# Optimization experiments

Measured on AMD Instinct MI355X. Metric: run time of the kernel, lower is better.

The kernel has to match this reference:

```python
import jax, jax.numpy as jnp
import numpy as np

N = 50000
E = 800000
NEG_SLOPE = 0.2  # PyG GATConv default


def _glorot(key, shape, scale=0.1):
    return jax.random.normal(key, shape, dtype=jnp.float32) * scale


def setup_inputs() -> dict:
    key = jax.random.key(0)
    ks = jax.random.split(key, 16)
    X = jax.random.normal(ks[0], (N, 128), dtype=jnp.float32)
    edge_index = jax.random.randint(ks[1], (2, E), 0, N, dtype=jnp.int64)
    edge_weight = jax.random.uniform(ks[2], (E,), dtype=jnp.float32)
    # GATConv layer params: W [in,out], att_src/att_dst [out], bias [out]
    W1, as1, ad1, b1 = _glorot(ks[3], (128, 128)), _glorot(ks[4], (128,)), _glorot(ks[5], (128,)), jnp.zeros((128,), jnp.float32)
    W2, as2, ad2, b2 = _glorot(ks[6], (128, 64)), _glorot(ks[7], (64,)), _glorot(ks[8], (64,)), jnp.zeros((64,), jnp.float32)
    W3, as3, ad3, b3 = _glorot(ks[9], (64, 32)), _glorot(ks[10], (32,)), _glorot(ks[11], (32,)), jnp.zeros((32,), jnp.float32)
    Wl, bl = _glorot(ks[12], (32, 1)), jnp.zeros((1,), jnp.float32)
    return {"X": X, "edge_index": edge_index, "edge_weight": edge_weight,
            "W1": W1, "as1": as1, "ad1": ad1, "b1": b1,
            "W2": W2, "as2": as2, "ad2": ad2, "b2": b2,
            "W3": W3, "as3": as3, "ad3": ad3, "b3": b3,
            "Wl": Wl, "bl": bl}


def gat_layer(x, src, dst, W, a_src, a_dst, b):
    # x: [N, in] -> h: [N, out]
    h = x @ W
    # per-node attention logits, gathered per edge
    alpha = jax.nn.leaky_relu((h * a_src).sum(-1)[src] + (h * a_dst).sum(-1)[dst], NEG_SLOPE)  # [E']
    # segment-softmax over incoming edges of each dst node
    amax = jax.ops.segment_max(alpha, dst, num_segments=N)
    ex = jnp.exp(alpha - amax[dst])
    denom = jax.ops.segment_sum(ex, dst, num_segments=N)
    w = ex / (denom[dst] + 1e-16)
    # scatter-add weighted messages
    out = jax.ops.segment_sum(h[src] * w[:, None], dst, num_segments=N)
    return out + b


def reference(X, edge_index, edge_weight, W1, as1, ad1, b1, W2, as2, ad2, b2, W3, as3, ad3, b3, Wl, bl):
    # GATConv add_self_loops=True: append self loops (static shape)
    loops = jnp.arange(N, dtype=edge_index.dtype)
    src = jnp.concatenate([edge_index[0], loops])
    dst = jnp.concatenate([edge_index[1], loops])
    # edge_weight is ignored by PyG GATConv when edge_dim is None (faithful)
    x = jax.nn.elu(gat_layer(X, src, dst, W1, as1, ad1, b1))
    x = jax.nn.elu(gat_layer(x, src, dst, W2, as2, ad2, b2))
    x = jax.nn.elu(gat_layer(x, src, dst, W3, as3, ad3, b3))
    x = x @ Wl + bl
    return jax.nn.sigmoid(x)[:, 0]
```

## Files before the change

kernel.cpp:

```cpp
#include <hip/hip_runtime.h>
#include <hip/hip_bf16.h>

typedef __attribute__((ext_vector_type(8))) short bf16x8;
typedef __attribute__((ext_vector_type(4))) float f32x4;

constexpr int NBMAX = 128;
constexpr int EPB   = 2048;
constexpr int CAP   = 12288;


__device__ __forceinline__ float bf2f(unsigned short u) {
    union { unsigned int i; float f; } c; c.i = ((unsigned int)u) << 16; return c.f;
}
__device__ __forceinline__ unsigned short f2bf(float f) {
    union { unsigned int i; float f; } c; c.f = f;
    unsigned int i = c.i;
    unsigned int r = (i + 0x7FFFu + ((i >> 16) & 1u)) >> 16;
    return (unsigned short)r;
}


__device__ __forceinline__ void pack_one(const float* __restrict__ W, int K, int OUT, int idx,
                                         unsigned short* __restrict__ hi, unsigned short* __restrict__ lo) {
    int KS = K >> 5;
    int lane = idx & 63;
    int rest = idx >> 6;
    int ks = rest % KS, ct = rest / KS;
    int m = lane & 15, kg = lane >> 4;
    size_t base = (size_t)idx * 8;
#pragma unroll
    for (int j = 0; j < 8; ++j) {
        float w = W[(size_t)(ks * 32 + kg * 8 + j) * OUT + ct * 16 + m];
        unsigned short h = f2bf(w);
        hi[base + j] = h;
        lo[base + j] = f2bf(w - bf2f(h));
    }
}

__global__ void pack_init(const float* __restrict__ W1, unsigned short* hi1, unsigned short* lo1,
                          const float* __restrict__ W2, unsigned short* hi2, unsigned short* lo2,
                          const float* __restrict__ W3, unsigned short* hi3, unsigned short* lo3,
                          int* __restrict__ cursor, int nb) {
    if (blockIdx.x < 13) {
        int idx = blockIdx.x * 256 + threadIdx.x;
        if (idx < 2048)               pack_one(W1, 128, 128, idx, hi1, lo1);
        else if (idx < 2048 + 1024)   pack_one(W2, 128,  64, idx - 2048, hi2, lo2);
        else if (idx < 2048 + 1280)   pack_one(W3,  64,  32, idx - 3072, hi3, lo3);
    } else {
        int t = threadIdx.x;
        if (t < nb) cursor[t] = t * CAP;
    }
}


__global__ __launch_bounds__(256) void bin_passA(const int* __restrict__ ei, int E, int N, int nb,
                                                 int* __restrict__ cursor,
                                                 unsigned int* __restrict__ stageG) {
    __shared__ int bcnt[NBMAX], bofs[NBMAX], gbase[NBMAX], bfill[NBMAX];
    __shared__ unsigned int stage[EPB];
    const int t = threadIdx.x;
    const int Et = E + N;
    const int e0 = blockIdx.x * EPB;
    const int ecnt = min(EPB, Et - e0);
    if (t < nb) { bcnt[t] = 0; bfill[t] = 0; }
    __syncthreads();
    unsigned int pk[8];
#pragma unroll
    for (int k = 0; k < 8; ++k) {
        int e = e0 + t + k * 256;
        pk[k] = 0xFFFFFFFFu;
        if (e < Et) {
            int s, d;
            if (e < E) { s = ei[e]; d = ei[E + e]; } else { s = d = e - E; }
            pk[k] = ((unsigned int)d << 16) | (unsigned int)s;
            atomicAdd(&bcnt[d >> 9], 1);
        }
    }
    __syncthreads();
    if (t == 0) {
        int run = 0;
        for (int i = 0; i < nb; ++i) { bofs[i] = run; run += bcnt[i]; }
    }
    __syncthreads();
    if (t < nb && bcnt[t] > 0) gbase[t] = atomicAdd(&cursor[t], bcnt[t]);
    __syncthreads();
#pragma unroll
    for (int k = 0; k < 8; ++k) {
        if (pk[k] != 0xFFFFFFFFu) {
            int b = pk[k] >> 25;
            int pos = bofs[b] + atomicAdd(&bfill[b], 1);
            stage[pos] = pk[k];
        }
    }
    __syncthreads();
    for (int i = t; i < ecnt; i += 256) {
        unsigned int p = stage[i];
        int b = p >> 25;
        stageG[(size_t)gbase[b] + (i - bofs[b])] = p;
    }
}


template <int K, int OUT>
__device__ __forceinline__ void gemm_body(const float* __restrict__ X,
                                          const unsigned short* __restrict__ Whi,
                                          const unsigned short* __restrict__ Wlo,
                                          const float* __restrict__ avs,
                                          const float* __restrict__ avd,
                                          unsigned short* __restrict__ Hb,
                                          float* __restrict__ asrc,
                                          float* __restrict__ adst, int N, int waveIdx) {
    constexpr int CT = OUT / 16, KS = K / 32;
    const int lane = threadIdx.x & 63;
    const int row0 = waveIdx << 4;
    if (row0 >= N) return;
    const int m = lane & 15, kg = lane >> 4;
    f32x4 acc[CT];
#pragma unroll
    for (int c = 0; c < CT; ++c) acc[c] = (f32x4){0.f, 0.f, 0.f, 0.f};
    const float* xrow = X + (size_t)(row0 + m) * K + kg * 8;
    const bf16x8* whf = (const bf16x8*)Whi;
    const bf16x8* wlf = (const bf16x8*)Wlo;
#pragma unroll
    for (int ks = 0; ks < KS; ++ks) {
        float4 x0 = *reinterpret_cast<const float4*>(xrow + ks * 32);
        float4 x1 = *reinterpret_cast<const float4*>(xrow + ks * 32 + 4);
        float xv[8] = {x0.x, x0.y, x0.z, x0.w, x1.x, x1.y, x1.z, x1.w};
        bf16x8 xhi, xlo;
#pragma unroll
        for (int j = 0; j < 8; ++j) {
            unsigned short h = f2bf(xv[j]);
            xhi[j] = (short)h;
            xlo[j] = (short)f2bf(xv[j] - bf2f(h));
        }
#pragma unroll
        for (int c = 0; c < CT; ++c) {
            bf16x8 wh = whf[(c * KS + ks) * 64 + lane];
            bf16x8 wl = wlf[(c * KS + ks) * 64 + lane];
            acc[c] = __builtin_amdgcn_mfma_f32_16x16x32_bf16(wh, xhi, acc[c], 0, 0, 0);
            acc[c] = __builtin_amdgcn_mfma_f32_16x16x32_bf16(wl, xhi, acc[c], 0, 0, 0);
            acc[c] = __builtin_amdgcn_mfma_f32_16x16x32_bf16(wh, xlo, acc[c], 0, 0, 0);
        }
    }
    float s = 0.f, d = 0.f;
    const size_t hbase = (size_t)(row0 + m) * OUT;
#pragma unroll
    for (int c = 0; c < CT; ++c) {
        const int col = c * 16 + kg * 4;
        float4 av = *reinterpret_cast<const float4*>(avs + col);
        float4 dv = *reinterpret_cast<const float4*>(avd + col);
        s += acc[c][0] * av.x + acc[c][1] * av.y + acc[c][2] * av.z + acc[c][3] * av.w;
        d += acc[c][0] * dv.x + acc[c][1] * dv.y + acc[c][2] * dv.z + acc[c][3] * dv.w;
        uint2 u;
        u.x = (unsigned int)f2bf(acc[c][0]) | ((unsigned int)f2bf(acc[c][1]) << 16);
        u.y = (unsigned int)f2bf(acc[c][2]) | ((unsigned int)f2bf(acc[c][3]) << 16);
        *reinterpret_cast<uint2*>(Hb + hbase + col) = u;
    }
    s += __shfl_xor(s, 16); s += __shfl_xor(s, 32);
    d += __shfl_xor(d, 16); d += __shfl_xor(d, 32);
    if (lane < 16) { asrc[row0 + lane] = s; adst[row0 + lane] = d; }
}


template <int K, int OUT>
__global__ __launch_bounds__(256) void gemm_attn_bf16(const unsigned short* __restrict__ Xb,
                                                      const unsigned short* __restrict__ Whi,
                                                      const unsigned short* __restrict__ Wlo,
                                                      const float* __restrict__ avs,
                                                      const float* __restrict__ avd,
                                                      unsigned short* __restrict__ Hb,
                                                      float* __restrict__ asrc,
                                                      float* __restrict__ adst, int N) {
    constexpr int CT = OUT / 16, KS = K / 32;
    const int lane = threadIdx.x & 63;
    const int row0 = (blockIdx.x * 4 + (threadIdx.x >> 6)) << 4;
    if (row0 >= N) return;
    const int m = lane & 15, kg = lane >> 4;
    f32x4 acc[CT];
#pragma unroll
    for (int c = 0; c < CT; ++c) acc[c] = (f32x4){0.f, 0.f, 0.f, 0.f};
    const unsigned short* xrow = Xb + (size_t)(row0 + m) * K + kg * 8;
    const bf16x8* whf = (const bf16x8*)Whi;
    const bf16x8* wlf = (const bf16x8*)Wlo;
#pragma unroll
    for (int ks = 0; ks < KS; ++ks) {
        bf16x8 x = *reinterpret_cast<const bf16x8*>(xrow + ks * 32);
#pragma unroll
        for (int c = 0; c < CT; ++c) {
            bf16x8 wh = whf[(c * KS + ks) * 64 + lane];
            bf16x8 wl = wlf[(c * KS + ks) * 64 + lane];
            acc[c] = __builtin_amdgcn_mfma_f32_16x16x32_bf16(wh, x, acc[c], 0, 0, 0);
            acc[c] = __builtin_amdgcn_mfma_f32_16x16x32_bf16(wl, x, acc[c], 0, 0, 0);
        }
    }
    float s = 0.f, d = 0.f;
    const size_t hbase = (size_t)(row0 + m) * OUT;
#pragma unroll
    for (int c = 0; c < CT; ++c) {
        const int col = c * 16 + kg * 4;
        float4 av = *reinterpret_cast<const float4*>(avs + col);
        float4 dv = *reinterpret_cast<const float4*>(avd + col);
        s += acc[c][0] * av.x + acc[c][1] * av.y + acc[c][2] * av.z + acc[c][3] * av.w;
        d += acc[c][0] * dv.x + acc[c][1] * dv.y + acc[c][2] * dv.z + acc[c][3] * dv.w;
        uint2 u;
        u.x = (unsigned int)f2bf(acc[c][0]) | ((unsigned int)f2bf(acc[c][1]) << 16);
        u.y = (unsigned int)f2bf(acc[c][2]) | ((unsigned int)f2bf(acc[c][3]) << 16);
        *reinterpret_cast<uint2*>(Hb + hbase + col) = u;
    }
    s += __shfl_xor(s, 16); s += __shfl_xor(s, 32);
    d += __shfl_xor(d, 16); d += __shfl_xor(d, 32);
    if (lane < 16) { asrc[row0 + lane] = s; adst[row0 + lane] = d; }
}


__global__ __launch_bounds__(512) void passB_gemm1(int nb, const int* __restrict__ cursor,
                                                   const unsigned int* __restrict__ stageG,
                                                   int* __restrict__ rowptr,
                                                   unsigned short* __restrict__ csrc,
                                                   int Et, int N,
                                                   const float* __restrict__ X,
                                                   const unsigned short* __restrict__ Whi,
                                                   const unsigned short* __restrict__ Wlo,
                                                   const float* __restrict__ avs,
                                                   const float* __restrict__ avd,
                                                   unsigned short* __restrict__ Hb,
                                                   float* __restrict__ asrc,
                                                   float* __restrict__ adst) {
    if ((int)blockIdx.x >= nb) {
        gemm_body<128, 128>(X, Whi, Wlo, avs, avd, Hb, asrc, adst, N,
                            (blockIdx.x - nb) * 8 + (threadIdx.x >> 6));
        return;
    }
    __shared__ int cnt[512], sofs[512], cnt2[512];
    __shared__ int tot[NBMAX];
    __shared__ unsigned short cs[CAP];
    __shared__ int rowbase_s, total_s;
    const int b = blockIdx.x, t = threadIdx.x;
    if (t < nb) tot[t] = cursor[t] - t * CAP;
    cnt[t] = 0; cnt2[t] = 0;
    __syncthreads();
    if (t == 0) {
        int run = 0;
        for (int i = 0; i < b; ++i) run += tot[i];
        rowbase_s = run; total_s = tot[b];
    }
    __syncthreads();
    const int tB = total_s, rb = rowbase_s;
    const unsigned int* sg = stageG + (size_t)b * CAP;
    for (int i = t; i < tB; i += 512) atomicAdd(&cnt[(sg[i] >> 16) & 511], 1);
    __syncthreads();
    int v = cnt[t];
    sofs[t] = v;
    __syncthreads();
    for (int off = 1; off < 512; off <<= 1) {
        int x = (t >= off) ? sofs[t - off] : 0;
        __syncthreads();
        sofs[t] += x;
        __syncthreads();
    }
    const int excl = sofs[t] - v;
    const int d = (b << 9) + t;
    if (d < N) rowptr[d] = rb + excl;
    if (b == nb - 1 && t == 0) rowptr[N] = Et;
    __syncthreads();
    sofs[t] = excl;
    __syncthreads();
    for (int i = t; i < tB; i += 512) {
        unsigned int p = sg[i];
        int ld = (p >> 16) & 511;
        int pos = sofs[ld] + atomicAdd(&cnt2[ld], 1);
        cs[pos] = (unsigned short)(p & 0xFFFFu);
    }
    __syncthreads();
    for (int i = t; i < tB; i += 512) csrc[rb + i] = cs[i];
}


template <int OUT, int MODE>
__global__ __launch_bounds__(256) void gat_aggregate(const unsigned short* __restrict__ Hb,
                                                     const float* __restrict__ asrc,
                                                     const float* __restrict__ adst,
                                                     const int* __restrict__ rowptr,
                                                     const unsigned short* __restrict__ csrc,
                                                     const float* __restrict__ bias,
                                                     unsigned short* __restrict__ Xout,
                                                     const float* __restrict__ Wl,
                                                     const float* __restrict__ bl,
                                                     float* __restrict__ fout, int N) {
    constexpr int SUBW = OUT / 4;
    constexpr int NPW = 64 / SUBW;
    __shared__ float2 pair[4][64];
    const int wslot = threadIdx.x >> 6;
    const int lane = threadIdx.x & 63;
    const int sub = lane / SUBW;
    const int sl  = lane % SUBW;
    const int wid = (blockIdx.x * blockDim.x + threadIdx.x) >> 6;
    const int node = wid * NPW + sub;
    if (node >= N) return;
    const int beg = rowptr[node], end = rowptr[node + 1];
    const float ad = adst[node];
    const int k4 = sl * 4;
    float a0 = 0.f, a1 = 0.f, a2 = 0.f, a3 = 0.f;
    float dpart = 0.f;
    for (int cbeg = beg; cbeg < end; cbeg += SUBW) {
        const int cnt = min(SUBW, end - cbeg);
        if (sl < cnt) {
            int s = csrc[cbeg + sl];
            float a = asrc[s] + ad;
            a = a > 0.f ? a : 0.2f * a;
            float u = __expf(a);
            dpart += u;
            pair[wslot][lane] = make_float2(u, __int_as_float(s));
        }
#pragma unroll 4
        for (int u = 0; u < cnt; ++u) {
            float2 p = pair[wslot][sub * SUBW + u];
            int s = __float_as_int(p.y);
            uint2 hu = *reinterpret_cast<const uint2*>(Hb + (size_t)s * OUT + k4);
            a0 += __uint_as_float(hu.x << 16) * p.x;
            a1 += __uint_as_float(hu.x & 0xffff0000u) * p.x;
            a2 += __uint_as_float(hu.y << 16) * p.x;
            a3 += __uint_as_float(hu.y & 0xffff0000u) * p.x;
        }
    }
#pragma unroll
    for (int off = SUBW / 2; off; off >>= 1) dpart += __shfl_xor(dpart, off);
    const float inv = 1.0f / (dpart + 1e-16f);
    float4 bi = *reinterpret_cast<const float4*>(bias + k4);
    float v0 = a0 * inv + bi.x, v1 = a1 * inv + bi.y;
    float v2 = a2 * inv + bi.z, v3 = a3 * inv + bi.w;
    v0 = v0 > 0.f ? v0 : expm1f(v0);
    v1 = v1 > 0.f ? v1 : expm1f(v1);
    v2 = v2 > 0.f ? v2 : expm1f(v2);
    v3 = v3 > 0.f ? v3 : expm1f(v3);
    if (MODE == 1) {
        float4 wl = *reinterpret_cast<const float4*>(Wl + k4);
        float part = v0 * wl.x + v1 * wl.y + v2 * wl.z + v3 * wl.w;
#pragma unroll
        for (int off = SUBW / 2; off; off >>= 1) part += __shfl_xor(part, off);
        if (sl == 0) fout[node] = 1.f / (1.f + __expf(-(part + bl[0])));
    } else {
        uint2 u;
        u.x = (unsigned int)f2bf(v0) | ((unsigned int)f2bf(v1) << 16);
        u.y = (unsigned int)f2bf(v2) | ((unsigned int)f2bf(v3) << 16);
        *reinterpret_cast<uint2*>(Xout + (size_t)node * OUT + k4) = u;
    }
}


extern "C" void kernel_launch(void* const* d_in, const int* in_sizes, int n_in,
                              void* d_out, int out_size, void* d_ws, size_t ws_size,
                              hipStream_t stream) {
    const float* X   = (const float*)d_in[0];
    const int*   ei  = (const int*)d_in[1];
    const float* W1  = (const float*)d_in[3];
    const float* a1s = (const float*)d_in[4];
    const float* a1d = (const float*)d_in[5];
    const float* b1  = (const float*)d_in[6];
    const float* W2  = (const float*)d_in[7];
    const float* a2s = (const float*)d_in[8];
    const float* a2d = (const float*)d_in[9];
    const float* b2  = (const float*)d_in[10];
    const float* W3  = (const float*)d_in[11];
    const float* a3s = (const float*)d_in[12];
    const float* a3d = (const float*)d_in[13];
    const float* b3  = (const float*)d_in[14];
    const float* Wl  = (const float*)d_in[15];
    const float* bl  = (const float*)d_in[16];
    float* out = (float*)d_out;

    const int N  = in_sizes[0] / 128;
    const int E  = in_sizes[1] / 2;
    const int Et = E + N;
    const int nb = (N + 511) >> 9;
    (void)n_in; (void)out_size; (void)ws_size;

    char* w = (char*)d_ws;
    size_t o = 0;
    auto alloc = [&](size_t bytes) -> void* {
        void* p = w + o;
        o += (bytes + 255) & ~(size_t)255;
        return p;
    };
    unsigned short* csrc = (unsigned short*)alloc((size_t)Et * 2);
    int*   rowptr   = (int*)alloc((size_t)(N + 1) * 4);
    int*   cursor   = (int*)alloc(NBMAX * 4);
    unsigned int* stageG = (unsigned int*)alloc((size_t)nb * CAP * 4);
    float* asrc     = (float*)alloc((size_t)N * 4);
    float* adst     = (float*)alloc((size_t)N * 4);
    unsigned short* Hb  = (unsigned short*)alloc((size_t)N * 128 * 2);
    unsigned short* XAb = (unsigned short*)alloc((size_t)N * 128 * 2);
    unsigned short* XBb = (unsigned short*)alloc((size_t)N * 64 * 2);
    unsigned short* whi1 = (unsigned short*)alloc(8 * 4 * 64 * 8 * 2);
    unsigned short* wlo1 = (unsigned short*)alloc(8 * 4 * 64 * 8 * 2);
    unsigned short* whi2 = (unsigned short*)alloc(4 * 4 * 64 * 8 * 2);
    unsigned short* wlo2 = (unsigned short*)alloc(4 * 4 * 64 * 8 * 2);
    unsigned short* whi3 = (unsigned short*)alloc(2 * 2 * 64 * 8 * 2);
    unsigned short* wlo3 = (unsigned short*)alloc(2 * 2 * 64 * 8 * 2);

    hipLaunchKernelGGL(pack_init, dim3(14), dim3(256), 0, stream,
                       W1, whi1, wlo1, W2, whi2, wlo2, W3, whi3, wlo3, cursor, nb);

    hipLaunchKernelGGL(bin_passA, dim3((Et + EPB - 1) / EPB), dim3(256), 0, stream,
                       ei, E, N, nb, cursor, stageG);

    const int gemmBlocks512 = (N + 127) / 128;
    hipLaunchKernelGGL(passB_gemm1, dim3(nb + gemmBlocks512), dim3(512), 0, stream,
                       nb, cursor, stageG, rowptr, csrc, Et, N,
                       X, whi1, wlo1, a1s, a1d, Hb, asrc, adst);

    hipLaunchKernelGGL((gat_aggregate<128, 0>), dim3((N + 7) / 8), dim3(256), 0, stream,
                       Hb, asrc, adst, rowptr, csrc, b1, XAb, nullptr, nullptr, nullptr, N);

    const int gemmBlocks = (N + 63) / 64;
    hipLaunchKernelGGL((gemm_attn_bf16<128, 64>), dim3(gemmBlocks), dim3(256), 0, stream,
                       XAb, whi2, wlo2, a2s, a2d, Hb, asrc, adst, N);
    hipLaunchKernelGGL((gat_aggregate<64, 0>), dim3((N + 15) / 16), dim3(256), 0, stream,
                       Hb, asrc, adst, rowptr, csrc, b2, XBb, nullptr, nullptr, nullptr, N);

    hipLaunchKernelGGL((gemm_attn_bf16<64, 32>), dim3(gemmBlocks), dim3(256), 0, stream,
                       XBb, whi3, wlo3, a3s, a3d, Hb, asrc, adst, N);
    hipLaunchKernelGGL((gat_aggregate<32, 1>), dim3((N + 31) / 32), dim3(256), 0, stream,
                       Hb, asrc, adst, rowptr, csrc, b3, nullptr, Wl, bl, out, N);
}
```

Baseline: 133.0 us.

## Replace atomic cursor binning with per-block count table and prefetch edge logits

Edge binning no longer uses global atomic cursors into fixed-capacity per-bin buffers. Each pass-A block now writes its locally sorted edges plus a per-bin count row, and pass-B blocks gather their bin's pieces from every pass-A block, using prefix scans to get offsets. Weight packing is folded into the pass-A launch, which removes one kernel launch. The large LDS staging buffer in pass-B is dropped in favour of direct global scatter into csrc. The aggregate kernels also software-prefetch the next chunk's source index and attention logit to hide gather latency. The trade-off is that pass-B now makes many small strided reads across hundreds of segments with mostly idle lanes, plus extra scan work.

```diff
diff --git a/kernel.cpp b/kernel.cpp
--- a/kernel.cpp
+++ b/kernel.cpp
@@ -6,7 +6,6 @@
 
 constexpr int NBMAX = 128;
 constexpr int EPB   = 2048;
-constexpr int CAP   = 12288;
 
 
 __device__ __forceinline__ float bf2f(unsigned short u) {
@@ -18,6 +17,8 @@
     unsigned int r = (i + 0x7FFFu + ((i >> 16) & 1u)) >> 16;
     return (unsigned short)r;
 }
+__device__ __forceinline__ float bflo(unsigned int u) { return __uint_as_float(u << 16); }
+__device__ __forceinline__ float bfhi(unsigned int u) { return __uint_as_float(u & 0xffff0000u); }
 
 
 __device__ __forceinline__ void pack_one(const float* __restrict__ W, int K, int OUT, int idx,
@@ -37,30 +38,26 @@
     }
 }
 
-__global__ void pack_init(const float* __restrict__ W1, unsigned short* hi1, unsigned short* lo1,
-                          const float* __restrict__ W2, unsigned short* hi2, unsigned short* lo2,
-                          const float* __restrict__ W3, unsigned short* hi3, unsigned short* lo3,
-                          int* __restrict__ cursor, int nb) {
+
+__global__ __launch_bounds__(256) void passA_pack(const int* __restrict__ ei, int E, int N, int nb, int nblkA,
+                                                  unsigned int* __restrict__ stageG,
+                                                  int* __restrict__ gcnt,
+                                                  const float* __restrict__ W1, unsigned short* hi1, unsigned short* lo1,
+                                                  const float* __restrict__ W2, unsigned short* hi2, unsigned short* lo2,
+                                                  const float* __restrict__ W3, unsigned short* hi3, unsigned short* lo3) {
     if (blockIdx.x < 13) {
         int idx = blockIdx.x * 256 + threadIdx.x;
         if (idx < 2048)               pack_one(W1, 128, 128, idx, hi1, lo1);
         else if (idx < 2048 + 1024)   pack_one(W2, 128,  64, idx - 2048, hi2, lo2);
         else if (idx < 2048 + 1280)   pack_one(W3,  64,  32, idx - 3072, hi3, lo3);
-    } else {
-        int t = threadIdx.x;
-        if (t < nb) cursor[t] = t * CAP;
-    }
-}
-
-
-__global__ __launch_bounds__(256) void bin_passA(const int* __restrict__ ei, int E, int N, int nb,
-                                                 int* __restrict__ cursor,
-                                                 unsigned int* __restrict__ stageG) {
-    __shared__ int bcnt[NBMAX], bofs[NBMAX], gbase[NBMAX], bfill[NBMAX];
+        return;
+    }
+    const int blk = blockIdx.x - 13;
+    __shared__ int bcnt[NBMAX], bofs[NBMAX], bfill[NBMAX];
     __shared__ unsigned int stage[EPB];
     const int t = threadIdx.x;
     const int Et = E + N;
-    const int e0 = blockIdx.x * EPB;
+    const int e0 = blk * EPB;
     const int ecnt = min(EPB, Et - e0);
     if (t < nb) { bcnt[t] = 0; bfill[t] = 0; }
     __syncthreads();
@@ -82,8 +79,6 @@
         for (int i = 0; i < nb; ++i) { bofs[i] = run; run += bcnt[i]; }
     }
     __syncthreads();
-    if (t < nb && bcnt[t] > 0) gbase[t] = atomicAdd(&cursor[t], bcnt[t]);
-    __syncthreads();
 #pragma unroll
     for (int k = 0; k < 8; ++k) {
         if (pk[k] != 0xFFFFFFFFu) {
@@ -93,11 +88,8 @@
         }
     }
     __syncthreads();
-    for (int i = t; i < ecnt; i += 256) {
-        unsigned int p = stage[i];
-        int b = p >> 25;
-        stageG[(size_t)gbase[b] + (i - bofs[b])] = p;
-    }
+    for (int i = t; i < ecnt; i += 256) stageG[(size_t)blk * EPB + i] = stage[i];
+    if (t < nb) gcnt[blk * nb + t] = bcnt[t];
 }
 
 
@@ -213,8 +205,9 @@
 }
 
 
-__global__ __launch_bounds__(512) void passB_gemm1(int nb, const int* __restrict__ cursor,
+__global__ __launch_bounds__(512) void passB_gemm1(int nb, int nblkA,
                                                    const unsigned int* __restrict__ stageG,
+                                                   const int* __restrict__ gcnt,
                                                    int* __restrict__ rowptr,
                                                    unsigned short* __restrict__ csrc,
                                                    int Et, int N,
@@ -231,29 +224,38 @@
                             (blockIdx.x - nb) * 8 + (threadIdx.x >> 6));
         return;
     }
+    __shared__ int offA[512], cntA[512], tmp[512];
     __shared__ int cnt[512], sofs[512], cnt2[512];
-    __shared__ int tot[NBMAX];
-    __shared__ unsigned short cs[CAP];
-    __shared__ int rowbase_s, total_s;
     const int b = blockIdx.x, t = threadIdx.x;
-    if (t < nb) tot[t] = cursor[t] - t * CAP;
+    int off = 0, c = 0;
+    if (t < nblkA) {
+        const int* g = gcnt + (size_t)t * nb;
+        for (int bb = 0; bb < b; ++bb) off += g[bb];
+        c = g[b];
+    }
+    offA[t] = off; cntA[t] = c;
     cnt[t] = 0; cnt2[t] = 0;
-    __syncthreads();
-    if (t == 0) {
-        int run = 0;
-        for (int i = 0; i < b; ++i) run += tot[i];
-        rowbase_s = run; total_s = tot[b];
-    }
-    __syncthreads();
-    const int tB = total_s, rb = rowbase_s;
-    const unsigned int* sg = stageG + (size_t)b * CAP;
-    for (int i = t; i < tB; i += 512) atomicAdd(&cnt[(sg[i] >> 16) & 511], 1);
+    tmp[t] = off;
+    __syncthreads();
+    for (int o2 = 1; o2 < 512; o2 <<= 1) {
+        int x = (t >= o2) ? tmp[t - o2] : 0;
+        __syncthreads();
+        tmp[t] += x;
+        __syncthreads();
+    }
+    const int rb = tmp[511];
+    const int wv = t >> 6, ln = t & 63;
+    for (int k = wv; k < nblkA; k += 8) {
+        const int cc = cntA[k];
+        const unsigned int* src = stageG + (size_t)k * EPB + offA[k];
+        for (int i = ln; i < cc; i += 64) atomicAdd(&cnt[(src[i] >> 16) & 511], 1);
+    }
     __syncthreads();
     int v = cnt[t];
     sofs[t] = v;
     __syncthreads();
-    for (int off = 1; off < 512; off <<= 1) {
-        int x = (t >= off) ? sofs[t - off] : 0;
+    for (int o2 = 1; o2 < 512; o2 <<= 1) {
+        int x = (t >= o2) ? sofs[t - o2] : 0;
         __syncthreads();
         sofs[t] += x;
         __syncthreads();
@@ -265,14 +267,16 @@
     __syncthreads();
     sofs[t] = excl;
     __syncthreads();
-    for (int i = t; i < tB; i += 512) {
-        unsigned int p = sg[i];
-        int ld = (p >> 16) & 511;
-        int pos = sofs[ld] + atomicAdd(&cnt2[ld], 1);
-        cs[pos] = (unsigned short)(p & 0xFFFFu);
-    }
-    __syncthreads();
-    for (int i = t; i < tB; i += 512) csrc[rb + i] = cs[i];
+    for (int k = wv; k < nblkA; k += 8) {
+        const int cc = cntA[k];
+        const unsigned int* src = stageG + (size_t)k * EPB + offA[k];
+        for (int i = ln; i < cc; i += 64) {
+            unsigned int p = src[i];
+            int ld = (p >> 16) & 511;
+            int pos = sofs[ld] + atomicAdd(&cnt2[ld], 1);
+            csrc[rb + pos] = (unsigned short)(p & 0xFFFFu);
+        }
+    }
 }
 
 
@@ -302,25 +306,27 @@
     const int k4 = sl * 4;
     float a0 = 0.f, a1 = 0.f, a2 = 0.f, a3 = 0.f;
     float dpart = 0.f;
+    int jl = beg + sl;
+    int s_nxt = 0; float l_nxt = 0.f;
+    if (jl < end) { s_nxt = csrc[jl]; l_nxt = asrc[s_nxt]; }
     for (int cbeg = beg; cbeg < end; cbeg += SUBW) {
         const int cnt = min(SUBW, end - cbeg);
         if (sl < cnt) {
-            int s = csrc[cbeg + sl];
-            float a = asrc[s] + ad;
+            float a = l_nxt + ad;
             a = a > 0.f ? a : 0.2f * a;
             float u = __expf(a);
             dpart += u;
-            pair[wslot][lane] = make_float2(u, __int_as_float(s));
-        }
+            pair[wslot][lane] = make_float2(u, __int_as_float(s_nxt));
+        }
+        jl = cbeg + SUBW + sl;
+        if (jl < end) { s_nxt = csrc[jl]; l_nxt = asrc[s_nxt]; }
 #pragma unroll 4
         for (int u = 0; u < cnt; ++u) {
             float2 p = pair[wslot][sub * SUBW + u];
             int s = __float_as_int(p.y);
             uint2 hu = *reinterpret_cast<const uint2*>(Hb + (size_t)s * OUT + k4);
-            a0 += __uint_as_float(hu.x << 16) * p.x;
-            a1 += __uint_as_float(hu.x & 0xffff0000u) * p.x;
-            a2 += __uint_as_float(hu.y << 16) * p.x;
-            a3 += __uint_as_float(hu.y & 0xffff0000u) * p.x;
+            a0 += bflo(hu.x) * p.x; a1 += bfhi(hu.x) * p.x;
+            a2 += bflo(hu.y) * p.x; a3 += bfhi(hu.y) * p.x;
         }
     }
 #pragma unroll
@@ -373,6 +379,7 @@
     const int E  = in_sizes[1] / 2;
     const int Et = E + N;
     const int nb = (N + 511) >> 9;
+    const int nblkA = (Et + EPB - 1) / EPB;
     (void)n_in; (void)out_size; (void)ws_size;
 
     char* w = (char*)d_ws;
@@ -384,8 +391,8 @@
     };
     unsigned short* csrc = (unsigned short*)alloc((size_t)Et * 2);
     int*   rowptr   = (int*)alloc((size_t)(N + 1) * 4);
-    int*   cursor   = (int*)alloc(NBMAX * 4);
-    unsigned int* stageG = (unsigned int*)alloc((size_t)nb * CAP * 4);
+    unsigned int* stageG = (unsigned int*)alloc((size_t)nblkA * EPB * 4);
+    int*   gcnt     = (int*)alloc((size_t)nblkA * nb * 4);
     float* asrc     = (float*)alloc((size_t)N * 4);
     float* adst     = (float*)alloc((size_t)N * 4);
     unsigned short* Hb  = (unsigned short*)alloc((size_t)N * 128 * 2);
@@ -398,15 +405,13 @@
     unsigned short* whi3 = (unsigned short*)alloc(2 * 2 * 64 * 8 * 2);
     unsigned short* wlo3 = (unsigned short*)alloc(2 * 2 * 64 * 8 * 2);
 
-    hipLaunchKernelGGL(pack_init, dim3(14), dim3(256), 0, stream,
-                       W1, whi1, wlo1, W2, whi2, wlo2, W3, whi3, wlo3, cursor, nb);
-
-    hipLaunchKernelGGL(bin_passA, dim3((Et + EPB - 1) / EPB), dim3(256), 0, stream,
-                       ei, E, N, nb, cursor, stageG);
+    hipLaunchKernelGGL(passA_pack, dim3(13 + nblkA), dim3(256), 0, stream,
+                       ei, E, N, nb, nblkA, stageG, gcnt,
+                       W1, whi1, wlo1, W2, whi2, wlo2, W3, whi3, wlo3);
 
     const int gemmBlocks512 = (N + 127) / 128;
     hipLaunchKernelGGL(passB_gemm1, dim3(nb + gemmBlocks512), dim3(512), 0, stream,
-                       nb, cursor, stageG, rowptr, csrc, Et, N,
+                       nb, nblkA, stageG, gcnt, rowptr, csrc, Et, N,
                        X, whi1, wlo1, a1s, a1d, Hb, asrc, adst);
 
     hipLaunchKernelGGL((gat_aggregate<128, 0>), dim3((N + 7) / 8), dim3(256), 0, stream,
```

Result: slower. 164.1 us (+23.4%).
